# Performance work log

Measured on AMD Instinct MI355X. Metric: run time of the kernel, lower is better.

The kernel has to match this reference:

```python
import jax, jax.numpy as jnp
import numpy as np

D_MODEL = 1024
N_HEADS = 16
HEAD_DIM = D_MODEL // N_HEADS


def setup_inputs() -> dict:
    key = jax.random.key(0)
    k1, k2, k3 = jax.random.split(key, 3)
    x = jax.random.normal(k1, (4, 2048, D_MODEL), dtype=jnp.float32)
    # per-head qkv Linear (bias=False): torch weight [3*head_dim, d_model];
    # store transposed and stacked over heads: [H, d_model, 3*head_dim]
    w_qkv = jax.random.normal(k2, (N_HEADS, D_MODEL, 3 * HEAD_DIM), dtype=jnp.float32) * (1.0 / np.sqrt(D_MODEL))
    # output Linear (bias=False), stored transposed: [d_model, d_model]
    w_out = jax.random.normal(k3, (D_MODEL, D_MODEL), dtype=jnp.float32) * (1.0 / np.sqrt(D_MODEL))
    return {"x": x, "w_qkv": w_qkv, "w_out": w_out}


def reference(x, w_qkv, w_out):
    hd = HEAD_DIM
    # all heads' qkv in one contraction: [B, H, S, 3*hd]
    qkv = jnp.einsum("bsd,hde->bhse", x, w_qkv)
    q, k, v = qkv[..., :hd], qkv[..., hd:2 * hd], qkv[..., 2 * hd:]
    scale = 1.0 / hd  # NOTE: original scales by 1/dk, not 1/sqrt(dk)
    scores = jnp.einsum("bhqe,bhke->bhqk", q, k) * scale
    attn = jax.nn.softmax(scores, axis=-1)
    z = jnp.einsum("bhqk,bhke->bhqe", attn, v)  # [B, H, S, hd]
    # concat heads along feature dim (head order = list order)
    b, h, s, _ = z.shape
    z = jnp.transpose(z, (0, 2, 1, 3)).reshape(b, s, h * hd)
    return z @ w_out
```

## Files before the change

kernel.cpp:

```cpp
#include <hip/hip_runtime.h>
#include <hip/hip_bf16.h>

typedef unsigned short u16;
typedef __attribute__((ext_vector_type(4))) float f32x4;
typedef __attribute__((ext_vector_type(16))) float f32x16;
typedef __attribute__((ext_vector_type(8))) short s16x8;
typedef __attribute__((ext_vector_type(4))) unsigned short u16x4;

static __device__ __forceinline__ u16 f32_to_bf16(float f) {
    union { float f; unsigned u; } v; v.f = f;
    unsigned r = v.u + 0x7FFF + ((v.u >> 16) & 1);
    return (u16)(r >> 16);
}

static __device__ __forceinline__ unsigned cvt_pk_bf16(float lo, float hi) {
    unsigned r;
    asm("v_cvt_pk_bf16_f32 %0, %1, %2" : "=v"(r) : "v"(lo), "v"(hi));
    return r;
}

static __device__ __forceinline__ void pswap2(unsigned &a, unsigned &b) {
#if defined(__has_builtin) && __has_builtin(__builtin_amdgcn_permlane32_swap)
    auto r = __builtin_amdgcn_permlane32_swap(a, b, false, false);
    a = r[0]; b = r[1];
#else
    asm volatile("v_permlane32_swap_b32 %0, %1" : "+v"(a), "+v"(b));
#endif
}

static __device__ __forceinline__ float xhalf_sum(float x) {
    unsigned a = __float_as_uint(x), b = a;
    pswap2(a, b);
    return __uint_as_float(a) + __uint_as_float(b);
}

static __device__ __forceinline__ float fexp2(float x) {
#if defined(__has_builtin) && __has_builtin(__builtin_amdgcn_exp2f)
    return __builtin_amdgcn_exp2f(x);
#else
    return exp2f(x);
#endif
}

#define GLOAD_LDS16(gptr, lptr) \
    __builtin_amdgcn_global_load_lds((const __attribute__((address_space(1))) void*)(gptr), \
                                     (__attribute__((address_space(3))) void*)(lptr), 16, 0, 0)

__global__ void cvt_all(const float* __restrict__ x, u16* __restrict__ xb,
                        const float* __restrict__ wq, u16* __restrict__ wqT,
                        const float* __restrict__ wo, u16* __restrict__ woT) {
    __shared__ float tile[32][33];
    const int bid = blockIdx.x;
    if (bid < 8192) {
        int i = (bid * 256 + threadIdx.x) * 4;
        f32x4 v = *(const f32x4*)(x + i);
        u16x4 o;
        o.x = f32_to_bf16(v.x); o.y = f32_to_bf16(v.y);
        o.z = f32_to_bf16(v.z); o.w = f32_to_bf16(v.w);
        *(u16x4*)(xb + i) = o;
    } else if (bid < 8192 + 3072) {
        const int b = bid - 8192;
        const int kb = b & 31, eb = (b >> 5) % 6, h = b / 192;
        const int xl = threadIdx.x & 31, y = threadIdx.x >> 5;
#pragma unroll
        for (int j = 0; j < 4; ++j) {
            int kl = y + j * 8;
            tile[kl][xl] = wq[((size_t)(h * 1024 + kb * 32 + kl)) * 192 + eb * 32 + xl];
        }
        __syncthreads();
#pragma unroll
        for (int j = 0; j < 4; ++j) {
            int el = y + j * 8;
            wqT[((size_t)(h * 192 + eb * 32 + el)) * 1024 + kb * 32 + xl] = f32_to_bf16(tile[xl][el]);
        }
    } else {
        const int b = bid - 8192 - 3072;
        const int kb = b & 31, nb = b >> 5;
        const int xl = threadIdx.x & 31, y = threadIdx.x >> 5;
#pragma unroll
        for (int j = 0; j < 4; ++j) {
            int kl = y + j * 8;
            tile[kl][xl] = wo[((size_t)(kb * 32 + kl)) * 1024 + nb * 32 + xl];
        }
        __syncthreads();
#pragma unroll
        for (int j = 0; j < 4; ++j) {
            int nl = y + j * 8;
            woT[((size_t)(nb * 32 + nl)) * 1024 + kb * 32 + xl] = f32_to_bf16(tile[xl][nl]);
        }
    }
}


#define SWZ4(r) (((r) & 3) ^ (((r) >> 2) & 3))

template <int EPI>
__global__ __launch_bounds__(256, 3)
void gemm_bt(const u16* __restrict__ A, const u16* __restrict__ B,
             float* __restrict__ Cf, u16* __restrict__ Qb, u16* __restrict__ Kb,
             u16* __restrict__ Vt, int M, int N, int K) {
    __shared__ __align__(16) u16 lA[3 * 128 * 32];
    __shared__ __align__(16) u16 lB[3 * 128 * 32];

    const int t = threadIdx.x;
    const int lane = t & 63;
    const int wave = t >> 6;
    const int wr = wave >> 1, wc = wave & 1;
    const int l15 = lane & 15, g = lane >> 4;

    const int nwg = gridDim.x;
    const int cpx = nwg >> 3;
    const int orig = blockIdx.x;
    const int logical = (orig & 7) * cpx + (orig >> 3);

    const int nbx = N >> 7;
    const int bx = logical % nbx, by = logical / nbx;
    const int bm = by << 7, bn = bx << 7;

    f32x4 acc[4][4] = {};

    const int sr0 = t >> 2;
    const int ss  = t & 3;

    const u16* Abase = A + (size_t)bm * K;
    const u16* Bbase = B + (size_t)bn * K;

    int aoff[4], boff[4];
#pragma unroll
    for (int i = 0; i < 4; ++i) {
        int ra = wr * 64 + i * 16 + l15;
        aoff[i] = (ra * 4 + (g ^ SWZ4(ra))) * 8;
        int rb = wc * 64 + i * 16 + l15;
        boff[i] = (rb * 4 + (g ^ SWZ4(rb))) * 8;
    }

#define GSTAGE(bb, kt) do { \
    _Pragma("unroll") \
    for (int c = 0; c < 2; ++c) { \
        int r = sr0 + 64 * c; \
        int cl = ss ^ SWZ4(r); \
        GLOAD_LDS16(Abase + (size_t)r * K + (kt) + cl * 8, &lA[(bb) + (r * 4 + ss) * 8]); \
        GLOAD_LDS16(Bbase + (size_t)r * K + (kt) + cl * 8, &lB[(bb) + (r * 4 + ss) * 8]); \
    } } while (0)

#define GEMM_STEP(B0, B2, KT, DO_STAGE, DO_SYNC, WAIT4)                        \
  {                                                                            \
    if (DO_STAGE) GSTAGE((B2) * 4096, (KT));                                   \
    s16x8 a0 = *(const s16x8*)&lA[(B0) * 4096 + aoff[0]];                      \
    s16x8 a1 = *(const s16x8*)&lA[(B0) * 4096 + aoff[1]];                      \
    s16x8 a2 = *(const s16x8*)&lA[(B0) * 4096 + aoff[2]];                      \
    s16x8 a3 = *(const s16x8*)&lA[(B0) * 4096 + aoff[3]];                      \
    s16x8 b0 = *(const s16x8*)&lB[(B0) * 4096 + boff[0]];                      \
    s16x8 b1 = *(const s16x8*)&lB[(B0) * 4096 + boff[1]];                      \
    s16x8 b2 = *(const s16x8*)&lB[(B0) * 4096 + boff[2]];                      \
    s16x8 b3 = *(const s16x8*)&lB[(B0) * 4096 + boff[3]];                      \
    acc[0][0] = __builtin_amdgcn_mfma_f32_16x16x32_bf16(b0, a0, acc[0][0], 0, 0, 0); \
    acc[0][1] = __builtin_amdgcn_mfma_f32_16x16x32_bf16(b1, a0, acc[0][1], 0, 0, 0); \
    acc[0][2] = __builtin_amdgcn_mfma_f32_16x16x32_bf16(b2, a0, acc[0][2], 0, 0, 0); \
    acc[0][3] = __builtin_amdgcn_mfma_f32_16x16x32_bf16(b3, a0, acc[0][3], 0, 0, 0); \
    acc[1][0] = __builtin_amdgcn_mfma_f32_16x16x32_bf16(b0, a1, acc[1][0], 0, 0, 0); \
    acc[1][1] = __builtin_amdgcn_mfma_f32_16x16x32_bf16(b1, a1, acc[1][1], 0, 0, 0); \
    acc[1][2] = __builtin_amdgcn_mfma_f32_16x16x32_bf16(b2, a1, acc[1][2], 0, 0, 0); \
    acc[1][3] = __builtin_amdgcn_mfma_f32_16x16x32_bf16(b3, a1, acc[1][3], 0, 0, 0); \
    acc[2][0] = __builtin_amdgcn_mfma_f32_16x16x32_bf16(b0, a2, acc[2][0], 0, 0, 0); \
    acc[2][1] = __builtin_amdgcn_mfma_f32_16x16x32_bf16(b1, a2, acc[2][1], 0, 0, 0); \
    acc[2][2] = __builtin_amdgcn_mfma_f32_16x16x32_bf16(b2, a2, acc[2][2], 0, 0, 0); \
    acc[2][3] = __builtin_amdgcn_mfma_f32_16x16x32_bf16(b3, a2, acc[2][3], 0, 0, 0); \
    acc[3][0] = __builtin_amdgcn_mfma_f32_16x16x32_bf16(b0, a3, acc[3][0], 0, 0, 0); \
    acc[3][1] = __builtin_amdgcn_mfma_f32_16x16x32_bf16(b1, a3, acc[3][1], 0, 0, 0); \
    acc[3][2] = __builtin_amdgcn_mfma_f32_16x16x32_bf16(b2, a3, acc[3][2], 0, 0, 0); \
    acc[3][3] = __builtin_amdgcn_mfma_f32_16x16x32_bf16(b3, a3, acc[3][3], 0, 0, 0); \
    if (DO_SYNC) {                                                             \
      if (WAIT4) { asm volatile("s_waitcnt vmcnt(4)" ::: "memory"); }          \
      else       { asm volatile("s_waitcnt vmcnt(0)" ::: "memory"); }          \
      __builtin_amdgcn_s_barrier();                                            \
      __builtin_amdgcn_sched_barrier(0);                                       \
    }                                                                          \
  }

    GSTAGE(0, 0);
    GSTAGE(4096, 32);
    asm volatile("s_waitcnt vmcnt(4)" ::: "memory");
    __builtin_amdgcn_s_barrier();
    __builtin_amdgcn_sched_barrier(0);

#pragma unroll 1
    for (int tt = 0; tt < 30; tt += 3) {
        GEMM_STEP(0, 2, (tt + 2) << 5, true, true, true);
        GEMM_STEP(1, 0, (tt + 3) << 5, true, true, true);
        GEMM_STEP(2, 1, (tt + 4) << 5, true, true, true);
    }
    GEMM_STEP(0, 0, 0, false, true, false);
    GEMM_STEP(1, 0, 0, false, false, false);
#undef GEMM_STEP
#undef GSTAGE

    if constexpr (EPI == 0) {
#pragma unroll
        for (int i = 0; i < 4; ++i) {
            int m = bm + wr * 64 + i * 16 + l15;
#pragma unroll
            for (int j = 0; j < 4; ++j) {
                int n0 = bn + wc * 64 + j * 16 + g * 4;
                *(f32x4*)&Cf[(size_t)m * N + n0] = acc[i][j];
            }
        }
    } else {
        const float qscale = 0.022542110013890054f;
#pragma unroll
        for (int j = 0; j < 4; ++j) {
            int n0 = bn + wc * 64 + j * 16 + g * 4;
            int h = n0 / 192;
            int e0 = n0 - h * 192;
#pragma unroll
            for (int i = 0; i < 4; ++i) {
                int m = bm + wr * 64 + i * 16 + l15;
                int bb = m >> 11, s = m & 2047;
                int bh = bb * 16 + h;
                if (e0 < 64) {
                    u16x4 q;
#pragma unroll
                    for (int r = 0; r < 4; ++r) q[r] = f32_to_bf16(acc[i][j][r] * qscale);
                    *(u16x4*)&Qb[((size_t)bh * 2048 + s) * 64 + e0] = q;
                } else if (e0 < 128) {
                    u16x4 kk;
#pragma unroll
                    for (int r = 0; r < 4; ++r) kk[r] = f32_to_bf16(acc[i][j][r]);
                    *(u16x4*)&Kb[((size_t)bh * 2048 + s) * 64 + (e0 - 64)] = kk;
                } else {
#pragma unroll
                    for (int r = 0; r < 4; ++r)
                        Vt[((size_t)bh * 64 + (e0 - 128 + r)) * 2048 + s] = f32_to_bf16(acc[i][j][r]);
                }
            }
        }
    }
}


static __device__ __forceinline__ void soft_pack(f32x16 p0, f32x16 p1, float& l,
                                                 s16x8& pv0, s16x8& pv1,
                                                 s16x8& pv2, s16x8& pv3) {
    float rs0 = 0.f, rs1 = 0.f, rs2 = 0.f, rs3 = 0.f;
#pragma unroll
    for (int r = 0; r < 16; r += 4) {
        p0[r]     = fexp2(p0[r]);     rs0 += p0[r];
        p0[r + 1] = fexp2(p0[r + 1]); rs1 += p0[r + 1];
        p0[r + 2] = fexp2(p0[r + 2]); rs2 += p0[r + 2];
        p0[r + 3] = fexp2(p0[r + 3]); rs3 += p0[r + 3];
        p1[r]     = fexp2(p1[r]);     rs0 += p1[r];
        p1[r + 1] = fexp2(p1[r + 1]); rs1 += p1[r + 1];
        p1[r + 2] = fexp2(p1[r + 2]); rs2 += p1[r + 2];
        p1[r + 3] = fexp2(p1[r + 3]); rs3 += p1[r + 3];
    }
    l += xhalf_sum((rs0 + rs1) + (rs2 + rs3));

    {
        unsigned c0 = cvt_pk_bf16(p0[0],  p0[1]);
        unsigned c1 = cvt_pk_bf16(p0[2],  p0[3]);
        unsigned c2 = cvt_pk_bf16(p0[4],  p0[5]);
        unsigned c3 = cvt_pk_bf16(p0[6],  p0[7]);
        unsigned c4 = cvt_pk_bf16(p0[8],  p0[9]);
        unsigned c5 = cvt_pk_bf16(p0[10], p0[11]);
        unsigned c6 = cvt_pk_bf16(p0[12], p0[13]);
        unsigned c7 = cvt_pk_bf16(p0[14], p0[15]);
        pswap2(c0, c2); pswap2(c1, c3);
        pswap2(c4, c6); pswap2(c5, c7);
        union { unsigned u[8]; s16x8 v[2]; } pa;
        pa.u[0] = c0; pa.u[1] = c1; pa.u[2] = c2; pa.u[3] = c3;
        pa.u[4] = c4; pa.u[5] = c5; pa.u[6] = c6; pa.u[7] = c7;
        pv0 = pa.v[0]; pv1 = pa.v[1];
    }
    {
        unsigned c0 = cvt_pk_bf16(p1[0],  p1[1]);
        unsigned c1 = cvt_pk_bf16(p1[2],  p1[3]);
        unsigned c2 = cvt_pk_bf16(p1[4],  p1[5]);
        unsigned c3 = cvt_pk_bf16(p1[6],  p1[7]);
        unsigned c4 = cvt_pk_bf16(p1[8],  p1[9]);
        unsigned c5 = cvt_pk_bf16(p1[10], p1[11]);
        unsigned c6 = cvt_pk_bf16(p1[12], p1[13]);
        unsigned c7 = cvt_pk_bf16(p1[14], p1[15]);
        pswap2(c0, c2); pswap2(c1, c3);
        pswap2(c4, c6); pswap2(c5, c7);
        union { unsigned u[8]; s16x8 v[2]; } pa;
        pa.u[0] = c0; pa.u[1] = c1; pa.u[2] = c2; pa.u[3] = c3;
        pa.u[4] = c4; pa.u[5] = c5; pa.u[6] = c6; pa.u[7] = c7;
        pv2 = pa.v[0]; pv3 = pa.v[1];
    }
}

__global__ __launch_bounds__(512, 4)
void attn32(const u16* __restrict__ Qb, const u16* __restrict__ Kb,
            const u16* __restrict__ Vt, u16* __restrict__ Zb) {
    __shared__ __align__(16) u16 lK[3 * 64 * 64];
    __shared__ __align__(16) u16 lV[3 * 64 * 64];
    __shared__ float lds_l[8][32];

    const int t = threadIdx.x;
    const int lane = t & 63;
    const int w = t >> 6;
    const int l31 = lane & 31, hi = lane >> 5;
    const int r7 = l31 & 7;

    const int orig = blockIdx.x;
    const int logical = (orig & 7) * 64 + (orig >> 3);
    const int bh = logical >> 3;
    const int qt = logical & 7;
    const int q0 = qt * 256 + w * 32;

    const u16* Kbh = Kb + (size_t)bh * 2048 * 64;
    const u16* Vbh = Vt + (size_t)bh * 64 * 2048;

    const int lr = lane >> 3;
    const int lc = (lane & 7) ^ lr;

    const u16* Qp = Qb + ((size_t)bh * 2048 + q0 + l31) * 64 + hi * 8;
    const s16x8 qf0 = *(const s16x8*)(Qp);
    const s16x8 qf1 = *(const s16x8*)(Qp + 16);
    const s16x8 qf2 = *(const s16x8*)(Qp + 32);
    const s16x8 qf3 = *(const s16x8*)(Qp + 48);

    const int ka0 = l31 * 64 + (((0 + hi) ^ r7) << 3);
    const int ka1 = l31 * 64 + (((2 + hi) ^ r7) << 3);
    const int ka2 = l31 * 64 + (((4 + hi) ^ r7) << 3);
    const int ka3 = l31 * 64 + (((6 + hi) ^ r7) << 3);

    f32x16 o0 = {}, o1 = {};
    float l = 0.f;

#define STAGE(bb, kvn) do { \
    int gr = w * 8 + lr; \
    GLOAD_LDS16(Kbh + (size_t)((kvn) + gr) * 64 + lc * 8, \
                &lK[(bb) + w * 512 + lane * 8]); \
    GLOAD_LDS16(Vbh + (size_t)gr * 2048 + (kvn) + lc * 8, \
                &lV[(bb) + w * 512 + lane * 8]); \
    } while (0)

#define ATTN_STEP(B0, B2, KVN, DO_STAGE, DO_SYNC, WAIT2)                             \
  {                                                                                  \
    if (DO_STAGE) STAGE((B2) * 4096, (KVN));                                         \
    f32x16 p0 = {}, p1 = {};                                                         \
    __builtin_amdgcn_s_setprio(1);                                                   \
    {                                                                                \
      s16x8 kf;                                                                      \
      kf = *(const s16x8*)&lK[(B0) * 4096 + ka0];                                    \
      p0 = __builtin_amdgcn_mfma_f32_32x32x16_bf16(kf, qf0, p0, 0, 0, 0);            \
      kf = *(const s16x8*)&lK[(B0) * 4096 + ka0 + 2048];                             \
      p1 = __builtin_amdgcn_mfma_f32_32x32x16_bf16(kf, qf0, p1, 0, 0, 0);            \
      kf = *(const s16x8*)&lK[(B0) * 4096 + ka1];                                    \
      p0 = __builtin_amdgcn_mfma_f32_32x32x16_bf16(kf, qf1, p0, 0, 0, 0);            \
      kf = *(const s16x8*)&lK[(B0) * 4096 + ka1 + 2048];                             \
      p1 = __builtin_amdgcn_mfma_f32_32x32x16_bf16(kf, qf1, p1, 0, 0, 0);            \
      kf = *(const s16x8*)&lK[(B0) * 4096 + ka2];                                    \
      p0 = __builtin_amdgcn_mfma_f32_32x32x16_bf16(kf, qf2, p0, 0, 0, 0);            \
      kf = *(const s16x8*)&lK[(B0) * 4096 + ka2 + 2048];                             \
      p1 = __builtin_amdgcn_mfma_f32_32x32x16_bf16(kf, qf2, p1, 0, 0, 0);            \
      kf = *(const s16x8*)&lK[(B0) * 4096 + ka3];                                    \
      p0 = __builtin_amdgcn_mfma_f32_32x32x16_bf16(kf, qf3, p0, 0, 0, 0);            \
      kf = *(const s16x8*)&lK[(B0) * 4096 + ka3 + 2048];                             \
      p1 = __builtin_amdgcn_mfma_f32_32x32x16_bf16(kf, qf3, p1, 0, 0, 0);            \
    }                                                                                \
    __builtin_amdgcn_s_setprio(0);                                                   \
    s16x8 pv0, pv1, pv2, pv3;                                                        \
    soft_pack(p0, p1, l, pv0, pv1, pv2, pv3);                                        \
    __builtin_amdgcn_s_setprio(1);                                                   \
    {                                                                                \
      s16x8 vf;                                                                      \
      vf = *(const s16x8*)&lV[(B0) * 4096 + ka0];                                    \
      o0 = __builtin_amdgcn_mfma_f32_32x32x16_bf16(pv0, vf, o0, 0, 0, 0);            \
      vf = *(const s16x8*)&lV[(B0) * 4096 + ka0 + 2048];                             \
      o1 = __builtin_amdgcn_mfma_f32_32x32x16_bf16(pv0, vf, o1, 0, 0, 0);            \
      vf = *(const s16x8*)&lV[(B0) * 4096 + ka1];                                    \
      o0 = __builtin_amdgcn_mfma_f32_32x32x16_bf16(pv1, vf, o0, 0, 0, 0);            \
      vf = *(const s16x8*)&lV[(B0) * 4096 + ka1 + 2048];                             \
      o1 = __builtin_amdgcn_mfma_f32_32x32x16_bf16(pv1, vf, o1, 0, 0, 0);            \
      vf = *(const s16x8*)&lV[(B0) * 4096 + ka2];                                    \
      o0 = __builtin_amdgcn_mfma_f32_32x32x16_bf16(pv2, vf, o0, 0, 0, 0);            \
      vf = *(const s16x8*)&lV[(B0) * 4096 + ka2 + 2048];                             \
      o1 = __builtin_amdgcn_mfma_f32_32x32x16_bf16(pv2, vf, o1, 0, 0, 0);            \
      vf = *(const s16x8*)&lV[(B0) * 4096 + ka3];                                    \
      o0 = __builtin_amdgcn_mfma_f32_32x32x16_bf16(pv3, vf, o0, 0, 0, 0);            \
      vf = *(const s16x8*)&lV[(B0) * 4096 + ka3 + 2048];                             \
      o1 = __builtin_amdgcn_mfma_f32_32x32x16_bf16(pv3, vf, o1, 0, 0, 0);            \
    }                                                                                \
    __builtin_amdgcn_s_setprio(0);                                                   \
    if (DO_SYNC) {                                                                   \
      if (WAIT2) { asm volatile("s_waitcnt vmcnt(2)" ::: "memory"); }                \
      else       { asm volatile("s_waitcnt vmcnt(0)" ::: "memory"); }                \
      __builtin_amdgcn_s_barrier();                                                  \
      __builtin_amdgcn_sched_barrier(0);                                             \
    }                                                                                \
  }

    STAGE(0, 0);
    STAGE(4096, 64);
    asm volatile("s_waitcnt vmcnt(2)" ::: "memory");
    __builtin_amdgcn_s_barrier();
    __builtin_amdgcn_sched_barrier(0);

#pragma unroll 1
    for (int tt = 0; tt < 30; tt += 3) {
        ATTN_STEP(0, 2, (tt + 2) << 6, true, true, true);
        ATTN_STEP(1, 0, (tt + 3) << 6, true, true, true);
        ATTN_STEP(2, 1, (tt + 4) << 6, true, true, true);
    }
    ATTN_STEP(0, 0, 0, false, true, false);
    ATTN_STEP(1, 0, 0, false, false, false);
#undef ATTN_STEP
#undef STAGE

    if (lane < 32) lds_l[w][l31] = l;
    __syncthreads();

    const int b = bh >> 4, h = bh & 15;
#pragma unroll
    for (int r = 0; r < 16; ++r) {
        int qrow = (r & 3) + 8 * (r >> 2) + 4 * hi;
        float inv = 1.0f / lds_l[w][qrow];
        size_t rowbase = ((size_t)(b * 2048 + q0 + qrow)) * 1024 + h * 64 + l31;
        Zb[rowbase]      = f32_to_bf16(o0[r] * inv);
        Zb[rowbase + 32] = f32_to_bf16(o1[r] * inv);
    }
}


extern "C" void kernel_launch(void* const* d_in, const int* in_sizes, int n_in,
                              void* d_out, int out_size, void* d_ws, size_t ws_size,
                              hipStream_t stream) {
    const float* x     = (const float*)d_in[0];
    const float* w_qkv = (const float*)d_in[1];
    const float* w_out = (const float*)d_in[2];
    float* out = (float*)d_out;

    char* ws = (char*)d_ws;
    u16* xb  = (u16*)ws; ws += (size_t)8192 * 1024 * 2;
    u16* wqT = (u16*)ws; ws += (size_t)3072 * 1024 * 2;
    u16* woT = (u16*)ws; ws += (size_t)1024 * 1024 * 2;
    u16* Qb  = (u16*)ws; ws += (size_t)64 * 2048 * 64 * 2;
    u16* Kb  = (u16*)ws; ws += (size_t)64 * 2048 * 64 * 2;
    u16* Vt  = (u16*)ws; ws += (size_t)64 * 2048 * 64 * 2;
    u16* Zb  = (u16*)ws; ws += (size_t)8192 * 1024 * 2;

    cvt_all<<<dim3(8192 + 3072 + 1024), dim3(256), 0, stream>>>(x, xb, w_qkv, wqT, w_out, woT);

    gemm_bt<1><<<dim3(64 * 24), dim3(256), 0, stream>>>(xb, wqT, nullptr, Qb, Kb, Vt,
                                                        8192, 3072, 1024);
    attn32<<<dim3(512), dim3(512), 0, stream>>>(Qb, Kb, Vt, Zb);
    gemm_bt<0><<<dim3(64 * 8), dim3(256), 0, stream>>>(Zb, woT, out, nullptr, nullptr, nullptr,
                                                       8192, 1024, 1024);
}
```

Before: 183.3 us.

## Shrink attention KV tile to 32 and use 4-wave blocks over 1024 workgroups

The attention kernel now processes 32 keys per step instead of 64 and uses 256-thread blocks covering 128 queries, launching 1024 workgroups. The V staging layout and swizzle are reworked for the 32-wide tiles, and softmax packing handles a single 32x32 score tile. The aim is more blocks for occupancy and load balance plus lower register and LDS pressure. In exchange it takes twice as many barrier-synchronised steps and spreads K/V reuse across fewer waves per block.

```diff
diff --git a/kernel.cpp b/kernel.cpp
--- a/kernel.cpp
+++ b/kernel.cpp
@@ -238,9 +238,8 @@
 }
 
 
-static __device__ __forceinline__ void soft_pack(f32x16 p0, f32x16 p1, float& l,
-                                                 s16x8& pv0, s16x8& pv1,
-                                                 s16x8& pv2, s16x8& pv3) {
+static __device__ __forceinline__ void soft_pack32(f32x16& p0, float& l,
+                                                   s16x8& pv0, s16x8& pv1) {
     float rs0 = 0.f, rs1 = 0.f, rs2 = 0.f, rs3 = 0.f;
 #pragma unroll
     for (int r = 0; r < 16; r += 4) {
@@ -248,53 +247,31 @@
         p0[r + 1] = fexp2(p0[r + 1]); rs1 += p0[r + 1];
         p0[r + 2] = fexp2(p0[r + 2]); rs2 += p0[r + 2];
         p0[r + 3] = fexp2(p0[r + 3]); rs3 += p0[r + 3];
-        p1[r]     = fexp2(p1[r]);     rs0 += p1[r];
-        p1[r + 1] = fexp2(p1[r + 1]); rs1 += p1[r + 1];
-        p1[r + 2] = fexp2(p1[r + 2]); rs2 += p1[r + 2];
-        p1[r + 3] = fexp2(p1[r + 3]); rs3 += p1[r + 3];
     }
     l += xhalf_sum((rs0 + rs1) + (rs2 + rs3));
 
-    {
-        unsigned c0 = cvt_pk_bf16(p0[0],  p0[1]);
-        unsigned c1 = cvt_pk_bf16(p0[2],  p0[3]);
-        unsigned c2 = cvt_pk_bf16(p0[4],  p0[5]);
-        unsigned c3 = cvt_pk_bf16(p0[6],  p0[7]);
-        unsigned c4 = cvt_pk_bf16(p0[8],  p0[9]);
-        unsigned c5 = cvt_pk_bf16(p0[10], p0[11]);
-        unsigned c6 = cvt_pk_bf16(p0[12], p0[13]);
-        unsigned c7 = cvt_pk_bf16(p0[14], p0[15]);
-        pswap2(c0, c2); pswap2(c1, c3);
-        pswap2(c4, c6); pswap2(c5, c7);
-        union { unsigned u[8]; s16x8 v[2]; } pa;
-        pa.u[0] = c0; pa.u[1] = c1; pa.u[2] = c2; pa.u[3] = c3;
-        pa.u[4] = c4; pa.u[5] = c5; pa.u[6] = c6; pa.u[7] = c7;
-        pv0 = pa.v[0]; pv1 = pa.v[1];
-    }
-    {
-        unsigned c0 = cvt_pk_bf16(p1[0],  p1[1]);
-        unsigned c1 = cvt_pk_bf16(p1[2],  p1[3]);
-        unsigned c2 = cvt_pk_bf16(p1[4],  p1[5]);
-        unsigned c3 = cvt_pk_bf16(p1[6],  p1[7]);
-        unsigned c4 = cvt_pk_bf16(p1[8],  p1[9]);
-        unsigned c5 = cvt_pk_bf16(p1[10], p1[11]);
-        unsigned c6 = cvt_pk_bf16(p1[12], p1[13]);
-        unsigned c7 = cvt_pk_bf16(p1[14], p1[15]);
-        pswap2(c0, c2); pswap2(c1, c3);
-        pswap2(c4, c6); pswap2(c5, c7);
-        union { unsigned u[8]; s16x8 v[2]; } pa;
-        pa.u[0] = c0; pa.u[1] = c1; pa.u[2] = c2; pa.u[3] = c3;
-        pa.u[4] = c4; pa.u[5] = c5; pa.u[6] = c6; pa.u[7] = c7;
-        pv2 = pa.v[0]; pv3 = pa.v[1];
-    }
-}
-
-__global__ __launch_bounds__(512, 4)
+    unsigned c0 = cvt_pk_bf16(p0[0],  p0[1]);
+    unsigned c1 = cvt_pk_bf16(p0[2],  p0[3]);
+    unsigned c2 = cvt_pk_bf16(p0[4],  p0[5]);
+    unsigned c3 = cvt_pk_bf16(p0[6],  p0[7]);
+    unsigned c4 = cvt_pk_bf16(p0[8],  p0[9]);
+    unsigned c5 = cvt_pk_bf16(p0[10], p0[11]);
+    unsigned c6 = cvt_pk_bf16(p0[12], p0[13]);
+    unsigned c7 = cvt_pk_bf16(p0[14], p0[15]);
+    pswap2(c0, c2); pswap2(c1, c3);
+    pswap2(c4, c6); pswap2(c5, c7);
+    union { unsigned u[8]; s16x8 v[2]; } pa;
+    pa.u[0] = c0; pa.u[1] = c1; pa.u[2] = c2; pa.u[3] = c3;
+    pa.u[4] = c4; pa.u[5] = c5; pa.u[6] = c6; pa.u[7] = c7;
+    pv0 = pa.v[0]; pv1 = pa.v[1];
+}
+
+__global__ __launch_bounds__(256, 4)
 void attn32(const u16* __restrict__ Qb, const u16* __restrict__ Kb,
             const u16* __restrict__ Vt, u16* __restrict__ Zb) {
-    __shared__ __align__(16) u16 lK[3 * 64 * 64];
-    __shared__ __align__(16) u16 lV[3 * 64 * 64];
-    __shared__ float lds_l[8][32];
+    __shared__ __align__(16) u16 lK[3 * 2048];
+    __shared__ __align__(16) u16 lV[3 * 2048];
+    __shared__ float lds_l[4][32];
 
     const int t = threadIdx.x;
     const int lane = t & 63;
@@ -303,16 +280,13 @@
     const int r7 = l31 & 7;
 
     const int orig = blockIdx.x;
-    const int logical = (orig & 7) * 64 + (orig >> 3);
-    const int bh = logical >> 3;
-    const int qt = logical & 7;
-    const int q0 = qt * 256 + w * 32;
+    const int logical = (orig & 7) * 128 + (orig >> 3);
+    const int bh = logical >> 4;
+    const int qt = logical & 15;
+    const int q0 = qt * 128 + w * 32;
 
     const u16* Kbh = Kb + (size_t)bh * 2048 * 64;
     const u16* Vbh = Vt + (size_t)bh * 64 * 2048;
-
-    const int lr = lane >> 3;
-    const int lc = (lane & 7) ^ lr;
 
     const u16* Qp = Qb + ((size_t)bh * 2048 + q0 + l31) * 64 + hi * 8;
     const s16x8 qf0 = *(const s16x8*)(Qp);
@@ -324,64 +298,52 @@
     const int ka1 = l31 * 64 + (((2 + hi) ^ r7) << 3);
     const int ka2 = l31 * 64 + (((4 + hi) ^ r7) << 3);
     const int ka3 = l31 * 64 + (((6 + hi) ^ r7) << 3);
+    const int s3  = (l31 >> 1) & 3;
+    const int va0 = l31 * 32 + (((0 + hi) ^ s3) << 3);
+    const int va1 = l31 * 32 + (((2 + hi) ^ s3) << 3);
 
     f32x16 o0 = {}, o1 = {};
     float l = 0.f;
 
 #define STAGE(bb, kvn) do { \
-    int gr = w * 8 + lr; \
-    GLOAD_LDS16(Kbh + (size_t)((kvn) + gr) * 64 + lc * 8, \
+    int kr_ = w * 8 + (lane >> 3); \
+    GLOAD_LDS16(Kbh + (size_t)((kvn) + kr_) * 64 + (((lane & 7) ^ (lane >> 3)) * 8), \
                 &lK[(bb) + w * 512 + lane * 8]); \
-    GLOAD_LDS16(Vbh + (size_t)gr * 2048 + (kvn) + lc * 8, \
+    int vr_ = w * 16 + (lane >> 2); \
+    GLOAD_LDS16(Vbh + (size_t)vr_ * 2048 + (kvn) + (((lane & 3) ^ ((lane >> 3) & 3)) * 8), \
                 &lV[(bb) + w * 512 + lane * 8]); \
     } while (0)
 
 #define ATTN_STEP(B0, B2, KVN, DO_STAGE, DO_SYNC, WAIT2)                             \
   {                                                                                  \
-    if (DO_STAGE) STAGE((B2) * 4096, (KVN));                                         \
-    f32x16 p0 = {}, p1 = {};                                                         \
+    if (DO_STAGE) STAGE((B2) * 2048, (KVN));                                         \
+    f32x16 p0 = {};                                                                  \
     __builtin_amdgcn_s_setprio(1);                                                   \
     {                                                                                \
       s16x8 kf;                                                                      \
-      kf = *(const s16x8*)&lK[(B0) * 4096 + ka0];                                    \
+      kf = *(const s16x8*)&lK[(B0) * 2048 + ka0];                                    \
       p0 = __builtin_amdgcn_mfma_f32_32x32x16_bf16(kf, qf0, p0, 0, 0, 0);            \
-      kf = *(const s16x8*)&lK[(B0) * 4096 + ka0 + 2048];                             \
-      p1 = __builtin_amdgcn_mfma_f32_32x32x16_bf16(kf, qf0, p1, 0, 0, 0);            \
-      kf = *(const s16x8*)&lK[(B0) * 4096 + ka1];                                    \
+      kf = *(const s16x8*)&lK[(B0) * 2048 + ka1];                                    \
       p0 = __builtin_amdgcn_mfma_f32_32x32x16_bf16(kf, qf1, p0, 0, 0, 0);            \
-      kf = *(const s16x8*)&lK[(B0) * 4096 + ka1 + 2048];                             \
-      p1 = __builtin_amdgcn_mfma_f32_32x32x16_bf16(kf, qf1, p1, 0, 0, 0);            \
-      kf = *(const s16x8*)&lK[(B0) * 4096 + ka2];                                    \
+      kf = *(const s16x8*)&lK[(B0) * 2048 + ka2];                                    \
       p0 = __builtin_amdgcn_mfma_f32_32x32x16_bf16(kf, qf2, p0, 0, 0, 0);            \
-      kf = *(const s16x8*)&lK[(B0) * 4096 + ka2 + 2048];                             \
-      p1 = __builtin_amdgcn_mfma_f32_32x32x16_bf16(kf, qf2, p1, 0, 0, 0);            \
-      kf = *(const s16x8*)&lK[(B0) * 4096 + ka3];                                    \
+      kf = *(const s16x8*)&lK[(B0) * 2048 + ka3];                                    \
       p0 = __builtin_amdgcn_mfma_f32_32x32x16_bf16(kf, qf3, p0, 0, 0, 0);            \
-      kf = *(const s16x8*)&lK[(B0) * 4096 + ka3 + 2048];                             \
-      p1 = __builtin_amdgcn_mfma_f32_32x32x16_bf16(kf, qf3, p1, 0, 0, 0);            \
     }                                                                                \
     __builtin_amdgcn_s_setprio(0);                                                   \
-    s16x8 pv0, pv1, pv2, pv3;                                                        \
-    soft_pack(p0, p1, l, pv0, pv1, pv2, pv3);                                        \
+    s16x8 pv0, pv1;                                                                  \
+    soft_pack32(p0, l, pv0, pv1);                                                    \
     __builtin_amdgcn_s_setprio(1);                                                   \
     {                                                                                \
       s16x8 vf;                                                                      \
-      vf = *(const s16x8*)&lV[(B0) * 4096 + ka0];                                    \
+      vf = *(const s16x8*)&lV[(B0) * 2048 + va0];                                    \
       o0 = __builtin_amdgcn_mfma_f32_32x32x16_bf16(pv0, vf, o0, 0, 0, 0);            \
-      vf = *(const s16x8*)&lV[(B0) * 4096 + ka0 + 2048];                             \
+      vf = *(const s16x8*)&lV[(B0) * 2048 + va0 + 1024];                             \
       o1 = __builtin_amdgcn_mfma_f32_32x32x16_bf16(pv0, vf, o1, 0, 0, 0);            \
-      vf = *(const s16x8*)&lV[(B0) * 4096 + ka1];                                    \
+      vf = *(const s16x8*)&lV[(B0) * 2048 + va1];                                    \
       o0 = __builtin_amdgcn_mfma_f32_32x32x16_bf16(pv1, vf, o0, 0, 0, 0);            \
-      vf = *(const s16x8*)&lV[(B0) * 4096 + ka1 + 2048];                             \
+      vf = *(const s16x8*)&lV[(B0) * 2048 + va1 + 1024];                             \
       o1 = __builtin_amdgcn_mfma_f32_32x32x16_bf16(pv1, vf, o1, 0, 0, 0);            \
-      vf = *(const s16x8*)&lV[(B0) * 4096 + ka2];                                    \
-      o0 = __builtin_amdgcn_mfma_f32_32x32x16_bf16(pv2, vf, o0, 0, 0, 0);            \
-      vf = *(const s16x8*)&lV[(B0) * 4096 + ka2 + 2048];                             \
-      o1 = __builtin_amdgcn_mfma_f32_32x32x16_bf16(pv2, vf, o1, 0, 0, 0);            \
-      vf = *(const s16x8*)&lV[(B0) * 4096 + ka3];                                    \
-      o0 = __builtin_amdgcn_mfma_f32_32x32x16_bf16(pv3, vf, o0, 0, 0, 0);            \
-      vf = *(const s16x8*)&lV[(B0) * 4096 + ka3 + 2048];                             \
-      o1 = __builtin_amdgcn_mfma_f32_32x32x16_bf16(pv3, vf, o1, 0, 0, 0);            \
     }                                                                                \
     __builtin_amdgcn_s_setprio(0);                                                   \
     if (DO_SYNC) {                                                                   \
@@ -393,19 +355,21 @@
   }
 
     STAGE(0, 0);
-    STAGE(4096, 64);
+    STAGE(2048, 32);
     asm volatile("s_waitcnt vmcnt(2)" ::: "memory");
     __builtin_amdgcn_s_barrier();
     __builtin_amdgcn_sched_barrier(0);
 
 #pragma unroll 1
-    for (int tt = 0; tt < 30; tt += 3) {
-        ATTN_STEP(0, 2, (tt + 2) << 6, true, true, true);
-        ATTN_STEP(1, 0, (tt + 3) << 6, true, true, true);
-        ATTN_STEP(2, 1, (tt + 4) << 6, true, true, true);
-    }
-    ATTN_STEP(0, 0, 0, false, true, false);
-    ATTN_STEP(1, 0, 0, false, false, false);
+    for (int tt = 0; tt < 60; tt += 3) {
+        ATTN_STEP(0, 2, (tt + 2) << 5, true, true, true);
+        ATTN_STEP(1, 0, (tt + 3) << 5, true, true, true);
+        ATTN_STEP(2, 1, (tt + 4) << 5, true, true, true);
+    }
+    ATTN_STEP(0, 2, 62 << 5, true, true, true);
+    ATTN_STEP(1, 0, 63 << 5, true, true, true);
+    ATTN_STEP(2, 0, 0, false, true, false);
+    ATTN_STEP(0, 0, 0, false, false, false);
 #undef ATTN_STEP
 #undef STAGE
 
@@ -445,7 +409,7 @@
 
     gemm_bt<1><<<dim3(64 * 24), dim3(256), 0, stream>>>(xb, wqT, nullptr, Qb, Kb, Vt,
                                                         8192, 3072, 1024);
-    attn32<<<dim3(512), dim3(512), 0, stream>>>(Qb, Kb, Vt, Zb);
+    attn32<<<dim3(1024), dim3(256), 0, stream>>>(Qb, Kb, Vt, Zb);
     gemm_bt<0><<<dim3(64 * 8), dim3(256), 0, stream>>>(Zb, woT, out, nullptr, nullptr, nullptr,
                                                        8192, 1024, 1024);
 }
```

New measurement: 193.0 us. 5.2% more time.
